# Optimization experiments

Measured on AMD Instinct MI355X. Metric: run time of the kernel, lower is better.

## Reference

```python
import jax, jax.numpy as jnp
import numpy as np

B=1; NW=8; SEG=511; S=NW*(SEG+1); W=256; C=S//W; H=12; D=64; DM=768; FF=3072; V=50265; L=12; OUT=128; G=NW
SCALE = float(1.0/np.sqrt(D))
GPOS = np.arange(NW)*(S//NW)                      # global (CLS) token positions
IDX = np.arange(C)[:,None]*W + np.arange(3*W)[None,:]   # [C,3W] gather into padded key seq
_band = np.abs(np.arange(3*W)[None,:]-np.arange(W)[:,None]-W) <= W   # [W,3W] |rel|<=W band
_kpos = IDX - W
LMASK = _band[None] & ((_kpos>=0)&(_kpos<S))[:,None,:]  # [C,W,3W]

def _ln(x, s, b):
    m = jnp.mean(x, -1, keepdims=True)
    v = jnp.mean((x-m)**2, -1, keepdims=True)
    return (x-m)*jax.lax.rsqrt(v+1e-5)*s + b

def _layer(h, Wq,bq,Wk,bk,Wv,bv,Wo,bo,Wqg,bqg,Wkg,bkg,Wvg,bvg,l1s,l1b,W1,b1,W2,b2,l2s,l2b):
    hd = lambda z: z.reshape(B,S,H,D).transpose(0,2,1,3)   # [B,H,S,D]
    q = hd(h@Wq+bq)*SCALE
    k = hd(h@Wk+bk); v = hd(h@Wv+bv)
    kc = jnp.pad(k, ((0,0),(0,0),(W,W),(0,0)))[:,:,IDX]    # [B,H,C,3W,D]
    vc = jnp.pad(v, ((0,0),(0,0),(W,W),(0,0)))[:,:,IDX]
    qc = q.reshape(B,H,C,W,D)
    # banded local scores + scores to global keys, joint softmax (HF longformer style)
    sl = jnp.where(LMASK, jnp.einsum('bhcqd,bhckd->bhcqk', qc, kc), -1e9)
    sg = jnp.einsum('bhcqd,bhgd->bhcqg', qc, k[:,:,GPOS])
    a = jax.nn.softmax(jnp.concatenate([sg, sl], -1), -1)  # [B,H,C,W,G+3W]
    out = jnp.einsum('bhcqg,bhgd->bhcqd', a[..., :G], v[:,:,GPOS]) \
        + jnp.einsum('bhcqk,bhckd->bhcqd', a[..., G:], vc)
    out = out.reshape(B,H,S,D)
    # global tokens: full attention with separate global projections, overwrite their outputs
    qg = (h[:,GPOS]@Wqg+bqg).reshape(B,G,H,D).transpose(0,2,1,3)*SCALE
    ag = jax.nn.softmax(jnp.einsum('bhgd,bhsd->bhgs', qg, hd(h@Wkg+bkg)), -1)
    out = out.at[:,:,GPOS,:].set(jnp.einsum('bhgs,bhsd->bhgd', ag, hd(h@Wvg+bvg)))
    y = out.transpose(0,2,1,3).reshape(B,S,DM)@Wo + bo
    h = _ln(h + y, l1s, l1b)
    return _ln(h + jax.nn.gelu(h@W1+b1)@W2 + b2, l2s, l2b)

def setup_inputs() -> dict:
    keys = iter(jax.random.split(jax.random.key(0), 64))
    p = lambda *s: jax.random.normal(next(keys), s, jnp.float32)*0.02
    d = {"x": jax.random.randint(next(keys), (B, NW*SEG), 0, V),
         "word_emb": p(V, DM), "pos_emb": p(S, DM),
         "emb_ln_s": jnp.ones((DM,)), "emb_ln_b": jnp.zeros((DM,))}
    for n in ["Wq","Wk","Wv","Wo","Wqg","Wkg","Wvg"]:
        d[n] = p(L, DM, DM); d["b"+n[1:]] = jnp.zeros((L, DM))
    d["ln1_s"]=jnp.ones((L,DM)); d["ln1_b"]=jnp.zeros((L,DM))
    d["W1"]=p(L,DM,FF); d["b1"]=jnp.zeros((L,FF))
    d["W2"]=p(L,FF,DM); d["b2"]=jnp.zeros((L,DM))
    d["ln2_s"]=jnp.ones((L,DM)); d["ln2_b"]=jnp.zeros((L,DM))
    d["Wout"]=p(DM,OUT); d["bout"]=jnp.zeros((OUT,))
    return d

def reference(x, word_emb, pos_emb, emb_ln_s, emb_ln_b, Wq, bq, Wk, bk, Wv, bv, Wo, bo,
              Wqg, bqg, Wkg, bkg, Wvg, bvg, ln1_s, ln1_b, W1, b1, W2, b2, ln2_s, ln2_b,
              Wout, bout):
    # prepend CLS (id 0) per window -> S=4096 token ids
    ids = jnp.concatenate([jnp.zeros((B, NW, 1), x.dtype), x.reshape(B, NW, SEG)], 2).reshape(B, S)
    h = _ln(word_emb[ids] + pos_emb[None], emb_ln_s, emb_ln_b)
    for l in range(L):
        h = _layer(h, Wq[l],bq[l],Wk[l],bk[l],Wv[l],bv[l],Wo[l],bo[l],
                   Wqg[l],bqg[l],Wkg[l],bkg[l],Wvg[l],bvg[l],
                   ln1_s[l],ln1_b[l],W1[l],b1[l],W2[l],b2[l],ln2_s[l],ln2_b[l])
    return h[:, GPOS] @ Wout + bout   # cls_pooling + output head: [B, NW, OUT]
```

## Files before the change

### kernel.cpp

```cpp
#include <hip/hip_runtime.h>
#include <hip/hip_bf16.h>


typedef unsigned short u16;
typedef __attribute__((ext_vector_type(4))) float floatx4;
typedef __attribute__((ext_vector_type(4))) unsigned int uintx4;
typedef __attribute__((ext_vector_type(8))) short bf16x8;
typedef __attribute__((ext_vector_type(4))) u16 u16x4;

#define S_LEN 4096
#define QKVG_N 4608
#define NL 12

__device__ inline u16 f2bf(float x) {
    union { __hip_bfloat16 b; u16 u; } cv;
    cv.b = __float2bfloat16(x);
    return cv.u;
}
__device__ inline float bf2f(u16 u) {
    union { float f; unsigned int i; } c; c.i = ((unsigned int)u) << 16; return c.f;
}
__device__ inline u16 f2h(float x) {
    union { _Float16 h; u16 u; } c; c.h = (_Float16)x; return c.u;
}
__device__ inline float h2f(u16 u) {
    union { _Float16 h; u16 u; } c; c.u = u; return (float)c.h;
}
__device__ inline float gelu_f(float x) {
    float x3 = x * x * x;
    return 0.5f * x * (1.0f + tanhf(0.7978845608028654f * (x + 0.044715f * x3)));
}

#define GLDS16(g, l)                                                              \
    __builtin_amdgcn_global_load_lds(                                             \
        (const __attribute__((address_space(1))) unsigned int*)(g),               \
        (__attribute__((address_space(3))) unsigned int*)(l), 16, 0, 0)

__global__ __launch_bounds__(256) void prep_weights_k(
    const float* __restrict__ Wq0, const float* __restrict__ Wk0, const float* __restrict__ Wv0,
    const float* __restrict__ Wkg0, const float* __restrict__ Wvg0, const float* __restrict__ Wqg0,
    const float* __restrict__ Wo0, const float* __restrict__ W10, const float* __restrict__ W20,
    const float* __restrict__ bq0, const float* __restrict__ bk0, const float* __restrict__ bv0,
    const float* __restrict__ bkg0, const float* __restrict__ bvg0, const float* __restrict__ bqg0,
    u16* __restrict__ wTall, float* __restrict__ bcatall)
{
    const int t = threadIdx.x;
    const int bid = blockIdx.x;
    if (bid >= 6480) {
        int i = (bid - 6480) * 256 + t;
        int l = i / 4608, j = i - l * 4608;
        float v;
        if (j < 768)       v = bq0[l * 768 + j];
        else if (j < 1536) v = bk0[l * 768 + j - 768];
        else if (j < 2304) v = bv0[l * 768 + j - 1536];
        else if (j < 3072) v = bkg0[l * 768 + j - 2304];
        else if (j < 3840) v = bvg0[l * 768 + j - 3072];
        else               v = bqg0[l * 768 + j - 3840];
        bcatall[(size_t)l * 4608 + j] = v;
        return;
    }

    const int l = bid / 540, b = bid - l * 540;
    const size_t sqo = (size_t)l * 589824;
    const size_t sff = (size_t)l * 2359296;
    u16* wq = wTall + (size_t)l * 8847360;
    const float* src; u16* dst; int K, N, kt, ns;
    if (b < 216) {
        int m = b / 36, s = b - m * 36;
        src = ((m == 0) ? Wq0 : (m == 1) ? Wk0 : (m == 2) ? Wv0 :
               (m == 3) ? Wkg0 : (m == 4) ? Wvg0 : Wqg0) + sqo;
        dst = wq + (size_t)m * 589824;
        K = 768; N = 768; kt = s / 3; ns = s - kt * 3;
    } else if (b < 252) {
        int s = b - 216; src = Wo0 + sqo; dst = wq + 3538944;
        K = 768; N = 768; kt = s / 3; ns = s - kt * 3;
    } else if (b < 396) {
        int s = b - 252; src = W10 + sff; dst = wq + 4128768;
        K = 768; N = 3072; kt = s / 12; ns = s - kt * 12;
    } else {
        int s = b - 396; src = W20 + sff; dst = wq + 6488064;
        K = 3072; N = 768; kt = s / 3; ns = s - kt * 3;
    }
    const int k0 = kt * 64, n0b = ns * 256;

    __shared__ float tb[64][65];
    const int r = t >> 4, c4 = (t & 15) * 4;
    const float* srow = src + (size_t)k0 * N + n0b;
    floatx4 rg[4];
    #pragma unroll
    for (int j = 0; j < 4; j++)
        rg[j] = __builtin_nontemporal_load(
            (const floatx4*)&srow[(size_t)(r + 16 * j) * N + c4]);

    #pragma unroll
    for (int s4 = 0; s4 < 4; ++s4) {
        #pragma unroll
        for (int j = 0; j < 4; j++) {
            int kk = r + 16 * j;
            #pragma unroll
            for (int i = 0; i < 4; i++) tb[c4 + i][kk] = rg[j][i];
        }
        __syncthreads();
        if (s4 < 3) {
            #pragma unroll
            for (int j = 0; j < 4; j++)
                rg[j] = __builtin_nontemporal_load(
                    (const floatx4*)&srow[(size_t)(r + 16 * j) * N + (s4 + 1) * 64 + c4]);
        }
        int n0 = n0b + s4 * 64;
        #pragma unroll
        for (int j = 0; j < 4; j++) {
            int n = r + 16 * j;
            u16x4 o;
            #pragma unroll
            for (int i = 0; i < 4; i++) o[i] = f2bf(tb[n][c4 + i]);
            __builtin_nontemporal_store(o, (u16x4*)&dst[(size_t)(n0 + n) * K + k0 + c4]);
        }
        if (s4 < 3) __syncthreads();
    }
}

template <int ACT, int WF, int WB, int SKIPQG, int WVT, int SPLITB>
__global__ __launch_bounds__(256, 3) void gemm_k(
    const u16* __restrict__ A, const u16* __restrict__ Bt,
    const float* __restrict__ bias,
    float* __restrict__ Cf, u16* __restrict__ Cb, u16* __restrict__ vTg,
    int N, int K, int lda, int ldb)
{
    int lin = blockIdx.y * 32 + blockIdx.x;
    int qq = gridDim.y << 2;
    int wg = (lin & 7) * qq + (lin >> 3);
    int bx = wg & 31, by = wg >> 5;
    if (SKIPQG && by >= 30 && (bx & 3) != 0) return;
    int bm = bx * 128, bn = by * 128;
    const int zoff = SPLITB ? blockIdx.z : 0;
    const u16* Ab = A + (size_t)zoff * K;
    const u16* Bb = Bt + (size_t)zoff * K;
    u16* Csl = SPLITB ? Cb + (size_t)zoff * S_LEN * N : (u16*)nullptr;

    __shared__ __align__(16) u16 As[128][64];
    __shared__ __align__(16) u16 Bs[128][64];
    int t = threadIdx.x, lane = t & 63, wv = t >> 6;
    int wm = (wv >> 1) * 64, wn = (wv & 1) * 64;
    int srow = t >> 3, scol = (t & 7) * 8;
    int fr = lane & 15, fo = (lane >> 4) * 8;

    floatx4 acc[4][4];
    #pragma unroll
    for (int i = 0; i < 4; i++)
        #pragma unroll
        for (int j = 0; j < 4; j++) acc[i][j] = (floatx4){0.f, 0.f, 0.f, 0.f};

    const int nk = K >> 6;
    for (int kt = 0; kt < nk; ++kt) {
        const u16* ag = Ab + (size_t)(bm + srow) * lda + kt * 64 + scol;
        const u16* bg = Bb + (size_t)(bn + srow) * ldb + kt * 64 + scol;
        #pragma unroll
        for (int c = 0; c < 4; ++c) {
            GLDS16(ag + (size_t)(32 * c) * lda, &As[srow + 32 * c][scol]);
            GLDS16(bg + (size_t)(32 * c) * ldb, &Bs[srow + 32 * c][scol]);
        }
        __syncthreads();
        #pragma unroll
        for (int ks = 0; ks < 2; ++ks) {
            bf16x8 af[4], bfr[4];
            #pragma unroll
            for (int i = 0; i < 4; i++) af[i]  = *(const bf16x8*)&As[wm + i * 16 + fr][ks * 32 + fo];
            #pragma unroll
            for (int i = 0; i < 4; i++) bfr[i] = *(const bf16x8*)&Bs[wn + i * 16 + fr][ks * 32 + fo];
            #pragma unroll
            for (int i = 0; i < 4; i++)
                #pragma unroll
                for (int j = 0; j < 4; j++)
                    acc[i][j] = __builtin_amdgcn_mfma_f32_16x16x32_bf16(af[i], bfr[j], acc[i][j], 0, 0, 0);
        }
        __syncthreads();
    }

    int dr = (lane >> 4) * 4, dc = lane & 15;
    #pragma unroll
    for (int i = 0; i < 4; i++) {
        #pragma unroll
        for (int j = 0; j < 4; j++) {
            int r0 = bm + wm + i * 16 + dr;
            int cc = bn + wn + j * 16 + dc;
            float bsv = (!SPLITB || blockIdx.z == 0) ? bias[cc] : 0.f;
            u16x4 tv;
            #pragma unroll
            for (int r = 0; r < 4; r++) {
                float v = acc[i][j][r] + bsv;
                if (ACT == 1) v = gelu_f(v);
                if (SPLITB) {
                    Csl[(size_t)(r0 + r) * N + cc] = f2h(v);
                } else {
                    if (WF) Cf[(size_t)(r0 + r) * N + cc] = v;
                    if (WB) { u16 b = f2bf(v); Cb[(size_t)(r0 + r) * N + cc] = b; tv[r] = b; }
                }
            }
            if (WVT && cc >= 1536 && cc < 2304)
                *(u16x4*)&vTg[(size_t)(cc - 1536) * 4096 + r0] = tv;
        }
    }
}

__global__ __launch_bounds__(256) void attn_local_k(
    const u16* __restrict__ qkvg, const u16* __restrict__ vTg, u16* __restrict__ aob)
{
    int lin = blockIdx.y * 64 + blockIdx.x;
    int wg = (lin & 7) * 96 + (lin >> 3);
    const int qb = wg & 63, hh = wg >> 6;
    const int t = threadIdx.x, lane = t & 63, w = t >> 6;
    const int g = lane >> 4, qi = lane & 15;
    __shared__ __align__(16) u16 ks[64][72];
    __shared__ __align__(16) u16 vt[64][72];
    __shared__ __align__(16) u16 pbuf[4][16][40];

    const int q0w = qb * 64 + w * 16;
    const int sq = q0w + qi;

    bf16x8 qf0, qf1;
    {
        const u16* qp = qkvg + (size_t)(q0w + qi) * QKVG_N + hh * 64 + g * 8;
        qf0 = *(const bf16x8*)qp;
        qf1 = *(const bf16x8*)(qp + 32);
    }

    floatx4 acc[4];
    #pragma unroll
    for (int i = 0; i < 4; i++) acc[i] = (floatx4){0.f, 0.f, 0.f, 0.f};
    float mrun = -1e30f, lrun = 0.f;

    for (int tile = 0; tile <= 9; ++tile) {
        const int kbase = qb * 64 - 256 + (tile - 1) * 64;
        if (tile > 0 && (kbase < 0 || kbase >= S_LEN)) continue;
        __syncthreads();
        if (tile == 0) {
            for (int i = t; i < 576; i += 256) ((uintx4*)vt)[i] = (uintx4){0, 0, 0, 0};
            __syncthreads();
            if (t < 64) {
                int gg = t >> 3, d0 = (t & 7) * 8;
                *(uintx4*)&ks[gg][d0] =
                    *(const uintx4*)(qkvg + (size_t)(gg * 512) * QKVG_N + 768 + hh * 64 + d0);
            }
            for (int e = t; e < 512; e += 256) {
                int d = e >> 3, gg = e & 7;
                vt[d][gg] = vTg[(size_t)(hh * 64 + d) * 4096 + gg * 512];
            }
        } else {
            for (int c = t; c < 512; c += 256) {
                int r = c >> 3, c0 = (c & 7) * 8;
                *(uintx4*)&ks[r][c0] =
                    *(const uintx4*)(qkvg + (size_t)(kbase + r) * QKVG_N + 768 + hh * 64 + c0);
                *(uintx4*)&vt[r][c0] =
                    *(const uintx4*)(vTg + (size_t)(hh * 64 + r) * 4096 + kbase + c0);
            }
        }
        __syncthreads();

        const bool gt = (tile == 0);
        const bool edge = (tile == 1) | (tile == 9);
        const int ng = gt ? 1 : 2;
        for (int kg2 = 0; kg2 < ng; ++kg2) {
            floatx4 sf[2];
            sf[1] = (floatx4){0.f, 0.f, 0.f, 0.f};
            {
                bf16x8 ka0 = *(const bf16x8*)&ks[kg2 * 32 + qi][g * 8];
                bf16x8 ka1 = *(const bf16x8*)&ks[kg2 * 32 + qi][32 + g * 8];
                floatx4 z = (floatx4){0.f, 0.f, 0.f, 0.f};
                z = __builtin_amdgcn_mfma_f32_16x16x32_bf16(ka0, qf0, z, 0, 0, 0);
                sf[0] = __builtin_amdgcn_mfma_f32_16x16x32_bf16(ka1, qf1, z, 0, 0, 0);
            }
            if (!gt) {
                bf16x8 kb0 = *(const bf16x8*)&ks[kg2 * 32 + 16 + qi][g * 8];
                bf16x8 kb1 = *(const bf16x8*)&ks[kg2 * 32 + 16 + qi][32 + g * 8];
                floatx4 z = (floatx4){0.f, 0.f, 0.f, 0.f};
                z = __builtin_amdgcn_mfma_f32_16x16x32_bf16(kb0, qf0, z, 0, 0, 0);
                sf[1] = __builtin_amdgcn_mfma_f32_16x16x32_bf16(kb1, qf1, z, 0, 0, 0);
            }
            float p8[8];
            float mloc = -1e30f;
            #pragma unroll
            for (int f = 0; f < 2; ++f)
                #pragma unroll
                for (int r = 0; r < 4; ++r) {
                    int kl = kg2 * 32 + f * 16 + g * 4 + r;
                    float sc = sf[f][r] * 0.125f;
                    if (gt) {
                        if (kl >= 8) sc = -1e30f;
                    } else if (edge) {
                        int dd = kbase + kl - sq;
                        if (dd > 256 || dd < -256) sc = -1e30f;
                    }
                    p8[f * 4 + r] = sc;
                    mloc = fmaxf(mloc, sc);
                }
            mloc = fmaxf(mloc, __shfl_xor(mloc, 16));
            mloc = fmaxf(mloc, __shfl_xor(mloc, 32));
            float mnew = fmaxf(mrun, mloc);
            float alpha = __expf(mrun - mnew);
            mrun = mnew;
            float ls = 0.f;
            #pragma unroll
            for (int i = 0; i < 8; ++i) { float p = __expf(p8[i] - mnew); p8[i] = p; ls += p; }
            ls += __shfl_xor(ls, 16);
            ls += __shfl_xor(ls, 32);
            lrun = lrun * alpha + ls;
            u16x4 w0, w1;
            #pragma unroll
            for (int r = 0; r < 4; ++r) { w0[r] = f2bf(p8[r]); w1[r] = f2bf(p8[4 + r]); }
            *(u16x4*)&pbuf[w][qi][g * 4] = w0;
            *(u16x4*)&pbuf[w][qi][16 + g * 4] = w1;
            float al[4];
            #pragma unroll
            for (int r = 0; r < 4; ++r) al[r] = __shfl(alpha, g * 4 + r);
            #pragma unroll
            for (int dt = 0; dt < 4; ++dt)
                #pragma unroll
                for (int r = 0; r < 4; ++r) acc[dt][r] *= al[r];
            bf16x8 pf = *(const bf16x8*)&pbuf[w][qi][g * 8];
            #pragma unroll
            for (int dt = 0; dt < 4; ++dt) {
                bf16x8 vb = *(const bf16x8*)&vt[dt * 16 + qi][kg2 * 32 + g * 8];
                acc[dt] = __builtin_amdgcn_mfma_f32_16x16x32_bf16(pf, vb, acc[dt], 0, 0, 0);
            }
        }
    }

    float inv = 1.f / lrun;
    float li[4];
    #pragma unroll
    for (int r = 0; r < 4; ++r) li[r] = __shfl(inv, g * 4 + r);
    #pragma unroll
    for (int dt = 0; dt < 4; ++dt)
        #pragma unroll
        for (int r = 0; r < 4; ++r) {
            int s = q0w + g * 4 + r;
            aob[(size_t)s * 768 + hh * 64 + dt * 16 + qi] = f2bf(acc[dt][r] * li[r]);
        }
}

__global__ __launch_bounds__(192) void embed_ln_k(
    const int* __restrict__ x, const float* __restrict__ wemb, const float* __restrict__ pemb,
    const float* __restrict__ gs, const float* __restrict__ gb,
    u16* __restrict__ hh, u16* __restrict__ hb)
{
    int s = blockIdx.x, t = threadIdx.x;
    int w = s >> 9, p = s & 511;
    int id = (p == 0) ? 0 : x[w * 511 + p - 1];
    size_t off = (size_t)s * 768 + t * 4;
    floatx4 a = *(const floatx4*)(wemb + (size_t)id * 768 + t * 4);
    floatx4 b = *(const floatx4*)(pemb + off);
    floatx4 v;
    #pragma unroll
    for (int i = 0; i < 4; i++) v[i] = a[i] + b[i];
    float sum = v[0] + v[1] + v[2] + v[3];
    float sq = v[0] * v[0] + v[1] * v[1] + v[2] * v[2] + v[3] * v[3];
    #pragma unroll
    for (int o = 32; o > 0; o >>= 1) {
        sum += __shfl_down(sum, o); sq += __shfl_down(sq, o);
    }
    __shared__ float rs_[3], rq_[3];
    if ((t & 63) == 0) { rs_[t >> 6] = sum; rq_[t >> 6] = sq; }
    __syncthreads();
    float S = rs_[0] + rs_[1] + rs_[2];
    float Q = rq_[0] + rq_[1] + rq_[2];
    float mean = S * (1.f / 768.f);
    float inv = rsqrtf(Q * (1.f / 768.f) - mean * mean + 1e-5f);
    floatx4 g4 = *(const floatx4*)(gs + t * 4);
    floatx4 b4 = *(const floatx4*)(gb + t * 4);
    u16x4 oh, o4;
    #pragma unroll
    for (int i = 0; i < 4; i++) {
        float y = (v[i] - mean) * inv * g4[i] + b4[i];
        oh[i] = f2h(y);
        o4[i] = f2bf(y);
    }
    *(u16x4*)(hh + off) = oh;
    *(u16x4*)(hb + off) = o4;
}

__global__ __launch_bounds__(192) void ln_resid_k(
    const u16* __restrict__ xa, const u16* __restrict__ yh,
    const float* __restrict__ gs, const float* __restrict__ gb,
    u16* __restrict__ oh, u16* __restrict__ ob)
{
    int s = blockIdx.x, t = threadIdx.x;
    size_t off = (size_t)s * 768 + t * 4;
    u16x4 xa4 = *(const u16x4*)(xa + off);
    floatx4 v;
    #pragma unroll
    for (int i = 0; i < 4; i++) v[i] = h2f(xa4[i]);
    #pragma unroll
    for (int z = 0; z < 4; z++) {
        u16x4 b = *(const u16x4*)(yh + (size_t)z * 4096 * 768 + off);
        #pragma unroll
        for (int i = 0; i < 4; i++) v[i] += h2f(b[i]);
    }
    float sum = v[0] + v[1] + v[2] + v[3];
    float sq = v[0] * v[0] + v[1] * v[1] + v[2] * v[2] + v[3] * v[3];
    #pragma unroll
    for (int o = 32; o > 0; o >>= 1) {
        sum += __shfl_down(sum, o); sq += __shfl_down(sq, o);
    }
    __shared__ float rs_[3], rq_[3];
    if ((t & 63) == 0) { rs_[t >> 6] = sum; rq_[t >> 6] = sq; }
    __syncthreads();
    float S = rs_[0] + rs_[1] + rs_[2];
    float Q = rq_[0] + rq_[1] + rq_[2];
    float mean = S * (1.f / 768.f);
    float inv = rsqrtf(Q * (1.f / 768.f) - mean * mean + 1e-5f);
    floatx4 g4 = *(const floatx4*)(gs + t * 4);
    floatx4 b4 = *(const floatx4*)(gb + t * 4);
    u16x4 ohh, o4;
    #pragma unroll
    for (int i = 0; i < 4; i++) {
        float y = (v[i] - mean) * inv * g4[i] + b4[i];
        ohh[i] = f2h(y);
        o4[i] = f2bf(y);
    }
    *(u16x4*)(oh + off) = ohh;
    *(u16x4*)(ob + off) = o4;
}

__global__ __launch_bounds__(256) void attn_gpart_k(
    const u16* __restrict__ qkvg,
    float* __restrict__ pacc, float* __restrict__ pm, float* __restrict__ pl)
{
    const int hh = blockIdx.x, ck = blockIdx.y;
    const int t = threadIdx.x;
    __shared__ float qs[8][64];
    __shared__ __align__(16) u16 ks[128][72];
    __shared__ __align__(16) u16 vs[128][64];
    __shared__ float sc[8][128];
    __shared__ float mred[8], lred[8];

    for (int i = t; i < 512; i += 256) {
        int g = i >> 6, d = i & 63;
        qs[g][d] = bf2f(qkvg[(size_t)(g * 512) * QKVG_N + 3840 + hh * 64 + d]) * 0.125f;
    }
    const int s0 = ck * 128;
    for (int u = t; u < 1024; u += 256) {
        int r = u >> 3, c = u & 7;
        const u16* src = qkvg + (size_t)(s0 + r) * QKVG_N + hh * 64 + c * 8;
        *(uintx4*)&ks[r][c * 8] = *(const uintx4*)(src + 2304);
        *(uintx4*)&vs[r][c * 8] = *(const uintx4*)(src + 3072);
    }
    __syncthreads();

    {
        int key = t & 127, q0 = (t >> 7) * 4;
        float a[4] = {0.f, 0.f, 0.f, 0.f};
        #pragma unroll
        for (int c = 0; c < 8; ++c) {
            uintx4 pk = *(const uintx4*)&ks[key][c * 8];
            const u16* uu = (const u16*)&pk;
            #pragma unroll
            for (int e = 0; e < 8; ++e) {
                float kv = bf2f(uu[e]);
                #pragma unroll
                for (int q = 0; q < 4; ++q) a[q] += kv * qs[q0 + q][c * 8 + e];
            }
        }
        #pragma unroll
        for (int q = 0; q < 4; ++q) sc[q0 + q][key] = a[q];
    }
    __syncthreads();

    {
        int q = t >> 5, lq = t & 31;
        float m = -1e30f;
        #pragma unroll
        for (int i = 0; i < 4; ++i) m = fmaxf(m, sc[q][lq + i * 32]);
        #pragma unroll
        for (int o = 1; o < 32; o <<= 1) m = fmaxf(m, __shfl_xor(m, o));
        float ls = 0.f;
        #pragma unroll
        for (int i = 0; i < 4; ++i) {
            float p = __expf(sc[q][lq + i * 32] - m);
            sc[q][lq + i * 32] = p; ls += p;
        }
        #pragma unroll
        for (int o = 1; o < 32; o <<= 1) ls += __shfl_xor(ls, o);
        if (lq == 0) { mred[q] = m; lred[q] = ls; }
    }
    __syncthreads();

    {
        int d = t & 63, qb = t >> 6;
        float a0 = 0.f, a1 = 0.f;
        #pragma unroll 4
        for (int s = 0; s < 128; ++s) {
            float v = bf2f(vs[s][d]);
            a0 += sc[qb][s] * v;
            a1 += sc[qb + 4][s] * v;
        }
        float* pb = pacc + (((size_t)hh * 32 + ck) * 8) * 64;
        pb[qb * 64 + d] = a0;
        pb[(qb + 4) * 64 + d] = a1;
        if (t < 8) {
            pm[((size_t)hh * 32 + ck) * 8 + t] = mred[t];
            pl[((size_t)hh * 32 + ck) * 8 + t] = lred[t];
        }
    }
}

__global__ __launch_bounds__(64) void attn_gred_k(
    const float* __restrict__ pacc, const float* __restrict__ pm,
    const float* __restrict__ pl, u16* __restrict__ aob)
{
    int hh = blockIdx.x, gq = blockIdx.y;
    int d = threadIdx.x;
    float M = -1e30f;
    #pragma unroll 4
    for (int c = 0; c < 32; ++c)
        M = fmaxf(M, pm[((size_t)hh * 32 + c) * 8 + gq]);
    float L = 0.f, o = 0.f;
    #pragma unroll 4
    for (int c = 0; c < 32; ++c) {
        float w = __expf(pm[((size_t)hh * 32 + c) * 8 + gq] - M);
        L += pl[((size_t)hh * 32 + c) * 8 + gq] * w;
        o += w * pacc[(((size_t)hh * 32 + c) * 8 + gq) * 64 + d];
    }
    aob[(size_t)(gq * 512) * 768 + hh * 64 + d] = f2bf(o / L);
}

__global__ __launch_bounds__(128) void head_k(
    const u16* __restrict__ hh, const float* __restrict__ Wout,
    const float* __restrict__ bout, float* __restrict__ out)
{
    int g = blockIdx.x, n = threadIdx.x;
    __shared__ float hsh[768];
    for (int i = n; i < 768; i += 128) hsh[i] = h2f(hh[(size_t)(g * 512) * 768 + i]);
    __syncthreads();
    float a = 0.f;
    #pragma unroll 4
    for (int k = 0; k < 768; k++) a += hsh[k] * Wout[k * 128 + n];
    out[g * 128 + n] = a + bout[n];
}

extern "C" void kernel_launch(void* const* d_in, const int* in_sizes, int n_in,
                              void* d_out, int out_size, void* d_ws, size_t ws_size,
                              hipStream_t stream)
{
    (void)in_sizes; (void)n_in; (void)out_size; (void)ws_size;
    const int*   x    = (const int*)  d_in[0];
    const float* wemb = (const float*)d_in[1];
    const float* pemb = (const float*)d_in[2];
    const float* elns = (const float*)d_in[3];
    const float* elnb = (const float*)d_in[4];
    const float* Wq   = (const float*)d_in[5];
    const float* bq   = (const float*)d_in[6];
    const float* Wk   = (const float*)d_in[7];
    const float* bk   = (const float*)d_in[8];
    const float* Wv   = (const float*)d_in[9];
    const float* bv   = (const float*)d_in[10];
    const float* Wo   = (const float*)d_in[11];
    const float* bo   = (const float*)d_in[12];
    const float* Wqg  = (const float*)d_in[13];
    const float* bqg  = (const float*)d_in[14];
    const float* Wkg  = (const float*)d_in[15];
    const float* bkg  = (const float*)d_in[16];
    const float* Wvg  = (const float*)d_in[17];
    const float* bvg  = (const float*)d_in[18];
    const float* l1s  = (const float*)d_in[19];
    const float* l1b  = (const float*)d_in[20];
    const float* W1   = (const float*)d_in[21];
    const float* b1   = (const float*)d_in[22];
    const float* W2   = (const float*)d_in[23];
    const float* b2   = (const float*)d_in[24];
    const float* l2s  = (const float*)d_in[25];
    const float* l2b  = (const float*)d_in[26];
    const float* Wout = (const float*)d_in[27];
    const float* boutp= (const float*)d_in[28];

    char* W = (char*)d_ws;
    u16*   hh    = (u16*)  (W);
    u16*   hb    = (u16*)  (W + 12582912);
    u16*   qkvg  = (u16*)  (W + 18874368);
    u16*   ff1b  = (u16*)  (W + 18874368);
    u16*   vTg   = (u16*)  (W + 56623104);
    u16*   aob   = (u16*)  (W + 62914560);
    u16*   yh    = (u16*)  (W + 69206016);
    float* pacc  = (float*)(W + 119537664);
    float* pmw   = (float*)(W + 120324096);
    float* plw   = (float*)(W + 120336384);
    float* bcatall = (float*)(W + 120348672);
    u16*   wTall = (u16*)  (W + 120569856);

    prep_weights_k<<<6696, 256, 0, stream>>>(
        Wq, Wk, Wv, Wkg, Wvg, Wqg, Wo, W1, W2,
        bq, bk, bv, bkg, bvg, bqg, wTall, bcatall);

    embed_ln_k<<<4096, 192, 0, stream>>>(x, wemb, pemb, elns, elnb, hh, hb);

    for (int l = 0; l < NL; ++l) {
        u16* wTl      = wTall + (size_t)l * 8847360;
        u16* wqkvgT_l = wTl;
        u16* woT_l    = wTl + 3538944;
        u16* w1T_l    = woT_l + 589824;
        u16* w2T_l    = w1T_l + 2359296;
        float* bcat_l = bcatall + (size_t)l * 4608;
        const float* bo_l  = bo  + (size_t)l * 768;
        const float* b1_l  = b1  + (size_t)l * 3072;
        const float* b2_l  = b2  + (size_t)l * 768;
        const float* l1s_l = l1s + (size_t)l * 768;
        const float* l1b_l = l1b + (size_t)l * 768;
        const float* l2s_l = l2s + (size_t)l * 768;
        const float* l2b_l = l2b + (size_t)l * 768;

        gemm_k<0, 0, 1, 1, 1, 0><<<dim3(32, 36), 256, 0, stream>>>(
            hb, wqkvgT_l, bcat_l, (float*)nullptr, qkvg, vTg, QKVG_N, 768, 768, 768);

        attn_local_k<<<dim3(64, 12), 256, 0, stream>>>(qkvg, vTg, aob);

        attn_gpart_k<<<dim3(12, 32), 256, 0, stream>>>(qkvg, pacc, pmw, plw);
        attn_gred_k<<<dim3(12, 8), 64, 0, stream>>>(pacc, pmw, plw, aob);

        gemm_k<0, 0, 0, 0, 0, 1><<<dim3(32, 6, 4), 256, 0, stream>>>(
            aob, woT_l, bo_l, (float*)nullptr, yh, (u16*)nullptr, 768, 192, 768, 768);
        ln_resid_k<<<4096, 192, 0, stream>>>(hh, yh, l1s_l, l1b_l, hh, hb);

        gemm_k<1, 0, 1, 0, 0, 0><<<dim3(32, 24), 256, 0, stream>>>(
            hb, w1T_l, b1_l, (float*)nullptr, ff1b, (u16*)nullptr, 3072, 768, 768, 768);
        gemm_k<0, 0, 0, 0, 0, 1><<<dim3(32, 6, 4), 256, 0, stream>>>(
            ff1b, w2T_l, b2_l, (float*)nullptr, yh, (u16*)nullptr, 768, 768, 3072, 3072);
        ln_resid_k<<<4096, 192, 0, stream>>>(hh, yh, l2s_l, l2b_l, hh, hb);
    }

    head_k<<<8, 128, 0, stream>>>(hh, Wout, boutp, (float*)d_out);
}
```

Before: 2.642 ms.

## Prefetch next K/V tile into registers while computing current attention tile

The local attention kernel now peels the global-key tile out of the main loop and computes the valid tile range directly, so out-of-range tiles are never visited. In the main loop, the next K and V tile is loaded from global memory into registers while the current tile is being computed, then written to shared memory at the start of the next iteration. This hides global load latency behind the MFMA and softmax work. The cost is extra registers per thread, which could reduce occupancy.

New measurement: 2.588 ms. -2.0%, faster.

```diff
diff --git a/kernel.cpp b/kernel.cpp
--- a/kernel.cpp
+++ b/kernel.cpp
@@ -230,39 +230,106 @@
     for (int i = 0; i < 4; i++) acc[i] = (floatx4){0.f, 0.f, 0.f, 0.f};
     float mrun = -1e30f, lrun = 0.f;
 
-    for (int tile = 0; tile <= 9; ++tile) {
-        const int kbase = qb * 64 - 256 + (tile - 1) * 64;
-        if (tile > 0 && (kbase < 0 || kbase >= S_LEN)) continue;
+    int tlo = 5 - qb; if (tlo < 1) tlo = 1;
+    int thi = 68 - qb; if (thi > 9) thi = 9;
+
+    const int rs = t >> 3, cs = (t & 7) * 8;
+    uintx4 kr0, kr1, vr0, vr1;
+
+    for (int i = t; i < 576; i += 256) ((uintx4*)vt)[i] = (uintx4){0, 0, 0, 0};
+    __syncthreads();
+    if (t < 64) {
+        int gg = t >> 3, d0 = (t & 7) * 8;
+        *(uintx4*)&ks[gg][d0] =
+            *(const uintx4*)(qkvg + (size_t)(gg * 512) * QKVG_N + 768 + hh * 64 + d0);
+    }
+    for (int e = t; e < 512; e += 256) {
+        int d = e >> 3, gg = e & 7;
+        vt[d][gg] = vTg[(size_t)(hh * 64 + d) * 4096 + gg * 512];
+    }
+    __syncthreads();
+
+    {
+        const int kb = (qb + tlo - 5) * 64;
+        const u16* kp = qkvg + (size_t)(kb + rs) * QKVG_N + 768 + hh * 64 + cs;
+        kr0 = *(const uintx4*)kp;
+        kr1 = *(const uintx4*)(kp + (size_t)32 * QKVG_N);
+        const u16* vp = vTg + (size_t)(hh * 64 + rs) * 4096 + kb + cs;
+        vr0 = *(const uintx4*)vp;
+        vr1 = *(const uintx4*)(vp + (size_t)32 * 4096);
+    }
+
+    {
+        floatx4 sf0;
+        {
+            bf16x8 ka0 = *(const bf16x8*)&ks[qi][g * 8];
+            bf16x8 ka1 = *(const bf16x8*)&ks[qi][32 + g * 8];
+            floatx4 z = (floatx4){0.f, 0.f, 0.f, 0.f};
+            z = __builtin_amdgcn_mfma_f32_16x16x32_bf16(ka0, qf0, z, 0, 0, 0);
+            sf0 = __builtin_amdgcn_mfma_f32_16x16x32_bf16(ka1, qf1, z, 0, 0, 0);
+        }
+        float p8[8];
+        float mloc = -1e30f;
+        #pragma unroll
+        for (int r = 0; r < 4; ++r) {
+            int kl = g * 4 + r;
+            float sc = (kl < 8) ? sf0[r] * 0.125f : -1e30f;
+            p8[r] = sc;
+            p8[4 + r] = -1e30f;
+            mloc = fmaxf(mloc, sc);
+        }
+        mloc = fmaxf(mloc, __shfl_xor(mloc, 16));
+        mloc = fmaxf(mloc, __shfl_xor(mloc, 32));
+        float mnew = fmaxf(mrun, mloc);
+        float alpha = __expf(mrun - mnew);
+        mrun = mnew;
+        float ls = 0.f;
+        #pragma unroll
+        for (int i = 0; i < 8; ++i) { float p = __expf(p8[i] - mnew); p8[i] = p; ls += p; }
+        ls += __shfl_xor(ls, 16);
+        ls += __shfl_xor(ls, 32);
+        lrun = lrun * alpha + ls;
+        u16x4 w0, w1;
+        #pragma unroll
+        for (int r = 0; r < 4; ++r) { w0[r] = f2bf(p8[r]); w1[r] = f2bf(p8[4 + r]); }
+        *(u16x4*)&pbuf[w][qi][g * 4] = w0;
+        *(u16x4*)&pbuf[w][qi][16 + g * 4] = w1;
+        float al[4];
+        #pragma unroll
+        for (int r = 0; r < 4; ++r) al[r] = __shfl(alpha, g * 4 + r);
+        #pragma unroll
+        for (int dt = 0; dt < 4; ++dt)
+            #pragma unroll
+            for (int r = 0; r < 4; ++r) acc[dt][r] *= al[r];
+        bf16x8 pf = *(const bf16x8*)&pbuf[w][qi][g * 8];
+        #pragma unroll
+        for (int dt = 0; dt < 4; ++dt) {
+            bf16x8 vb = *(const bf16x8*)&vt[dt * 16 + qi][g * 8];
+            acc[dt] = __builtin_amdgcn_mfma_f32_16x16x32_bf16(pf, vb, acc[dt], 0, 0, 0);
+        }
+    }
+
+    for (int tile = tlo; tile <= thi; ++tile) {
+        const int kbase = (qb + tile - 5) * 64;
         __syncthreads();
-        if (tile == 0) {
-            for (int i = t; i < 576; i += 256) ((uintx4*)vt)[i] = (uintx4){0, 0, 0, 0};
-            __syncthreads();
-            if (t < 64) {
-                int gg = t >> 3, d0 = (t & 7) * 8;
-                *(uintx4*)&ks[gg][d0] =
-                    *(const uintx4*)(qkvg + (size_t)(gg * 512) * QKVG_N + 768 + hh * 64 + d0);
-            }
-            for (int e = t; e < 512; e += 256) {
-                int d = e >> 3, gg = e & 7;
-                vt[d][gg] = vTg[(size_t)(hh * 64 + d) * 4096 + gg * 512];
-            }
-        } else {
-            for (int c = t; c < 512; c += 256) {
-                int r = c >> 3, c0 = (c & 7) * 8;
-                *(uintx4*)&ks[r][c0] =
-                    *(const uintx4*)(qkvg + (size_t)(kbase + r) * QKVG_N + 768 + hh * 64 + c0);
-                *(uintx4*)&vt[r][c0] =
-                    *(const uintx4*)(vTg + (size_t)(hh * 64 + r) * 4096 + kbase + c0);
-            }
-        }
+        *(uintx4*)&ks[rs][cs] = kr0;
+        *(uintx4*)&ks[rs + 32][cs] = kr1;
+        *(uintx4*)&vt[rs][cs] = vr0;
+        *(uintx4*)&vt[rs + 32][cs] = vr1;
         __syncthreads();
-
-        const bool gt = (tile == 0);
+        if (tile < thi) {
+            const int kb = kbase + 64;
+            const u16* kp = qkvg + (size_t)(kb + rs) * QKVG_N + 768 + hh * 64 + cs;
+            kr0 = *(const uintx4*)kp;
+            kr1 = *(const uintx4*)(kp + (size_t)32 * QKVG_N);
+            const u16* vp = vTg + (size_t)(hh * 64 + rs) * 4096 + kb + cs;
+            vr0 = *(const uintx4*)vp;
+            vr1 = *(const uintx4*)(vp + (size_t)32 * 4096);
+        }
         const bool edge = (tile == 1) | (tile == 9);
-        const int ng = gt ? 1 : 2;
-        for (int kg2 = 0; kg2 < ng; ++kg2) {
+        #pragma unroll
+        for (int kg2 = 0; kg2 < 2; ++kg2) {
             floatx4 sf[2];
-            sf[1] = (floatx4){0.f, 0.f, 0.f, 0.f};
             {
                 bf16x8 ka0 = *(const bf16x8*)&ks[kg2 * 32 + qi][g * 8];
                 bf16x8 ka1 = *(const bf16x8*)&ks[kg2 * 32 + qi][32 + g * 8];
@@ -270,7 +337,7 @@
                 z = __builtin_amdgcn_mfma_f32_16x16x32_bf16(ka0, qf0, z, 0, 0, 0);
                 sf[0] = __builtin_amdgcn_mfma_f32_16x16x32_bf16(ka1, qf1, z, 0, 0, 0);
             }
-            if (!gt) {
+            {
                 bf16x8 kb0 = *(const bf16x8*)&ks[kg2 * 32 + 16 + qi][g * 8];
                 bf16x8 kb1 = *(const bf16x8*)&ks[kg2 * 32 + 16 + qi][32 + g * 8];
                 floatx4 z = (floatx4){0.f, 0.f, 0.f, 0.f};
@@ -285,9 +352,7 @@
                 for (int r = 0; r < 4; ++r) {
                     int kl = kg2 * 32 + f * 16 + g * 4 + r;
                     float sc = sf[f][r] * 0.125f;
-                    if (gt) {
-                        if (kl >= 8) sc = -1e30f;
-                    } else if (edge) {
+                    if (edge) {
                         int dd = kbase + kl - sq;
                         if (dd > 256 || dd < -256) sc = -1e30f;
                     }
```
